# Optimization experiments

Hardware: AMD Instinct MI355X
Metric: run time of the kernel (lower is better)

The kernel has to match this reference:

```python
import jax, jax.numpy as jnp
import numpy as np

EMBED = 2048
HEADS = 32
HEAD_DIM = EMBED // HEADS
Q_BITS = 4
Q_MAX = 2 ** (Q_BITS - 1) - 1  # 7
DECOMP = 8
CHUNK = 256


def _sym_qdq(x, scale):
    # sym_quant followed by sym_dequant (float32 math, clamp to [-8, 7])
    s = jnp.clip(jnp.abs(scale), 1e-9, None)
    return jnp.clip(jnp.round(x / s), -(Q_MAX + 1), Q_MAX) * s


def _quant_weight(w):
    # per-output-channel symmetric int4 quant-dequant of weight [out, in]
    w = w.astype(jnp.float32)
    s = jnp.max(jnp.abs(w), axis=-1, keepdims=True) / Q_MAX
    return _sym_qdq(w, s)


def _chunk_decompose(x2d):
    """Tender chunked activation quantization.
    Splits rows into chunks of CHUNK, subtracts per-chunk channel bias,
    groups channels into DECOMP scale groups by their column max, and
    applies per-group int4 quant-dequant. Vectorized over the DECOMP groups
    (the masks partition channels, so a per-channel scale gather is exact).
    """
    T, H = x2d.shape
    chunks = (T + CHUNK - 1) // CHUNK
    pad = chunks * CHUNK - T
    xp = jnp.pad(x2d, ((0, pad), (0, 0))).reshape(chunks, CHUNK, H).astype(jnp.float32)
    ch_bias = (jnp.max(xp, axis=1, keepdims=True) + jnp.min(xp, axis=1, keepdims=True)) / 2
    xz = xp - ch_bias                                   # [chunks, CHUNK, H]
    tmax = jnp.max(jnp.abs(xz), axis=(1, 2))            # [chunks]
    cmax = jnp.max(jnp.abs(xz), axis=1)                 # [chunks, H]
    # thresholds t_i = tmax / 2^(DECOMP-1-i), ascending in i
    thr = tmax[:, None] / (2.0 ** jnp.arange(DECOMP - 1, -1, -1, dtype=jnp.float32))
    # group index: i=0 if cmax<=t0, else first i with t_{i-1} < cmax <= t_i
    idx = jnp.sum(cmax[:, :, None] > thr[:, None, : DECOMP - 1], axis=-1)  # [chunks, H]
    scale = tmax[:, None] / (2.0 ** (DECOMP - 1 - idx).astype(jnp.float32)) / Q_MAX
    result = _sym_qdq(xz, scale[:, None, :])            # [chunks, CHUNK, H]
    return result, ch_bias, T


def reference(hidden_states, q_weight, k_weight, v_weight, o_weight,
              q_bias, k_bias, v_bias, o_bias):
    bsz, tgt, H = hidden_states.shape
    # int4 dequantized weights, transposed for right-multiply
    WQ = _quant_weight(q_weight).T
    WK = _quant_weight(k_weight).T
    WV = _quant_weight(v_weight).T
    WO = _quant_weight(o_weight).T

    result, ch_bias, n = _chunk_decompose(hidden_states.reshape(bsz * tgt, H))

    def proj(w_orig, w_dq_t, b):
        # bias-corrected dequant GEMM: per-chunk channel bias uses the
        # ORIGINAL (fp) weight, quantized residual uses the int4 weight
        y = result @ w_dq_t + ch_bias @ w_orig.astype(jnp.float32).T
        return y.reshape(-1, H)[:n] + b

    scaling = HEAD_DIM ** -0.5
    Q = (proj(q_weight, WQ, q_bias) * scaling).reshape(bsz, tgt, HEADS, HEAD_DIM)
    K = proj(k_weight, WK, k_bias).reshape(bsz, tgt, HEADS, HEAD_DIM)
    V = proj(v_weight, WV, v_bias).reshape(bsz, tgt, HEADS, HEAD_DIM)

    # quant_mha == False path: plain attention
    attn = jnp.einsum('bqhd,bkhd->bhqk', Q, K)
    probs = jax.nn.softmax(attn, axis=-1)
    ctx = jnp.einsum('bhqk,bkhd->bqhd', probs, V).reshape(bsz * tgt, H)

    # output projection through the same chunked quant pipeline
    r2, cb2, n2 = _chunk_decompose(ctx)
    out = (r2 @ WO + cb2 @ o_weight.astype(jnp.float32).T).reshape(-1, H)[:n2] + o_bias
    return out.reshape(bsz, tgt, H)


def setup_inputs() -> dict:
    key = jax.random.key(0)
    ks = jax.random.split(key, 10)
    B, T = 2, 1024
    inp = {
        'hidden_states': jax.random.normal(ks[0], (B, T, EMBED), dtype=jnp.float32),
        'q_weight': jax.random.normal(ks[1], (EMBED, EMBED), dtype=jnp.float32) * 0.02,
        'k_weight': jax.random.normal(ks[2], (EMBED, EMBED), dtype=jnp.float32) * 0.02,
        'v_weight': jax.random.normal(ks[3], (EMBED, EMBED), dtype=jnp.float32) * 0.02,
        'o_weight': jax.random.normal(ks[4], (EMBED, EMBED), dtype=jnp.float32) * 0.02,
        'q_bias': jax.random.normal(ks[5], (EMBED,), dtype=jnp.float32) * 0.02,
        'k_bias': jax.random.normal(ks[6], (EMBED,), dtype=jnp.float32) * 0.02,
        'v_bias': jax.random.normal(ks[7], (EMBED,), dtype=jnp.float32) * 0.02,
        'o_bias': jax.random.normal(ks[8], (EMBED,), dtype=jnp.float32) * 0.02,
    }
    return inp
```

## Files before the change

kernel.cpp:

```cpp
#include <hip/hip_runtime.h>
#include <hip/hip_bf16.h>

typedef unsigned short u16;
typedef unsigned int u32;
typedef __attribute__((ext_vector_type(8))) short bs8;
typedef __attribute__((ext_vector_type(4))) float fx4;
typedef __attribute__((ext_vector_type(4))) float f4_t;
typedef __attribute__((ext_vector_type(4))) unsigned int u4_t;

#define HDIM 2048
#define NCH 8

__device__ inline u16 f2bf(float f) {
  __hip_bfloat16 h = __float2bfloat16(f);
  return __builtin_bit_cast(u16, h);
}
__device__ inline float bf2f(u16 u) {
  __hip_bfloat16 h = __builtin_bit_cast(__hip_bfloat16, u);
  return __bfloat162float(h);
}
__device__ inline float pow2i(int e) {
  return __builtin_bit_cast(float, (unsigned)((127 + e) << 23));
}
__device__ inline void gld_lds16(const void* g, void* l) {
  __builtin_amdgcn_global_load_lds((const __attribute__((address_space(1))) void*)g,
                                   (__attribute__((address_space(3))) void*)l, 16, 0, 0);
}

__global__ __launch_bounds__(256) void k_wquant_cbw(
    const float* __restrict__ w0, const float* __restrict__ w1,
    const float* __restrict__ w2, const float* __restrict__ bias,
    u16* __restrict__ wq, float* __restrict__ sw, float* __restrict__ cbw,
    int NC) {
  int o = blockIdx.x, t = threadIdx.x;
  const float* w = (o < 2048) ? w0 : ((o < 4096) ? w1 : w2);
  const float* wrow = w + (size_t)(o & 2047) * HDIM;
  const f4_t* row4 = (const f4_t*)wrow;
  f4_t x0 = row4[2 * t], x1 = row4[2 * t + 1];
  float am = 0.f;
#pragma unroll
  for (int j = 0; j < 4; j++) { am = fmaxf(am, fabsf(x0[j])); am = fmaxf(am, fabsf(x1[j])); }
#pragma unroll
  for (int m = 1; m < 64; m <<= 1) am = fmaxf(am, __shfl_xor(am, m));
  __shared__ float red[4];
  if ((t & 63) == 0) red[t >> 6] = am;
  __syncthreads();
  am = fmaxf(fmaxf(red[0], red[1]), fmaxf(red[2], red[3]));
  float s = fmaxf(am / 7.0f, 1e-9f);
  if (t == 0) sw[o] = s;
  bs8 ov;
#pragma unroll
  for (int j = 0; j < 4; j++) {
    float q0 = fminf(fmaxf(rintf(x0[j] / s), -8.f), 7.f);
    float q1 = fminf(fmaxf(rintf(x1[j] / s), -8.f), 7.f);
    ov[j]     = (short)f2bf(q0);
    ov[j + 4] = (short)f2bf(q1);
  }
  ((bs8*)(wq + (size_t)o * HDIM))[t] = ov;
  float acc[NCH];
#pragma unroll
  for (int c = 0; c < NCH; c++) {
    const f4_t* bc = (const f4_t*)(bias + (size_t)c * HDIM);
    f4_t b0 = bc[2 * t], b1 = bc[2 * t + 1];
    float a = 0.f;
#pragma unroll
    for (int j = 0; j < 4; j++) a += x0[j] * b0[j] + x1[j] * b1[j];
    acc[c] = a;
  }
  __shared__ float redc[NCH][4];
#pragma unroll
  for (int c = 0; c < NCH; c++) {
    float a = acc[c];
#pragma unroll
    for (int m = 1; m < 64; m <<= 1) a += __shfl_xor(a, m);
    if ((t & 63) == 0) redc[c][t >> 6] = a;
  }
  __syncthreads();
  if (t < NCH) cbw[t * NC + o] = redc[t][0] + redc[t][1] + redc[t][2] + redc[t][3];
}

__global__ __launch_bounds__(256) void k_stats(const float* __restrict__ x,
                                               float* __restrict__ biasO,
                                               float* __restrict__ cmaxO) {
  int ch = blockIdx.x >> 3;
  int c = ((blockIdx.x & 7) << 8) + threadIdx.x;
  const float* base = x + (size_t)ch * 256 * HDIM + c;
  float mx = -1e30f, mn = 1e30f;
  for (int r = 0; r < 256; r++) { float v = base[(size_t)r * HDIM]; mx = fmaxf(mx, v); mn = fminf(mn, v); }
  float bi = (mx + mn) * 0.5f;
  biasO[ch * HDIM + c] = bi;
  cmaxO[ch * HDIM + c] = fmaxf(mx - bi, bi - mn);
}

__global__ __launch_bounds__(256) void k_tscale(const float* __restrict__ cmax,
                                                float* __restrict__ scaleO,
                                                float* __restrict__ e2O,
                                                float* __restrict__ tcO) {
  int ch = blockIdx.x, t = threadIdx.x;
  const float* cr = cmax + ch * HDIM;
  float v[8];
  float mx = 0.f;
#pragma unroll
  for (int i = 0; i < 8; i++) { v[i] = cr[i * 256 + t]; mx = fmaxf(mx, v[i]); }
#pragma unroll
  for (int m = 1; m < 64; m <<= 1) mx = fmaxf(mx, __shfl_xor(mx, m));
  __shared__ float red[4];
  __shared__ float tms;
  if ((t & 63) == 0) red[t >> 6] = mx;
  __syncthreads();
  if (t == 0) tms = fmaxf(fmaxf(red[0], red[1]), fmaxf(red[2], red[3]));
  __syncthreads();
  float tmax = tms;
  if (t == 0) tcO[ch] = (tmax / 7.0f) * pow2i(-7);
#pragma unroll
  for (int i = 0; i < 8; i++) {
    int idx = 0;
#pragma unroll
    for (int k = 0; k < 7; k++) idx += (v[i] > tmax * pow2i(k - 7)) ? 1 : 0;
    float s = (tmax * pow2i(idx - 7)) / 7.0f;
    scaleO[ch * HDIM + i * 256 + t] = fmaxf(s, 1e-9f);
    e2O[ch * HDIM + i * 256 + t] = pow2i(idx);
  }
}

__global__ __launch_bounds__(256) void k_qdq(const float* __restrict__ x,
                                             const float* __restrict__ bias,
                                             const float* __restrict__ scale,
                                             const float* __restrict__ e2,
                                             u16* __restrict__ out) {
  int row = blockIdx.x, t = threadIdx.x;
  int ch = row >> 8;
  const f4_t* xr = (const f4_t*)(x + (size_t)row * HDIM);
  const f4_t* br = (const f4_t*)(bias + (size_t)ch * HDIM);
  const f4_t* sr = (const f4_t*)(scale + (size_t)ch * HDIM);
  const f4_t* er = (const f4_t*)(e2 + (size_t)ch * HDIM);
  f4_t x0 = xr[2 * t], x1 = xr[2 * t + 1];
  f4_t b0 = br[2 * t], b1 = br[2 * t + 1];
  f4_t s0 = sr[2 * t], s1 = sr[2 * t + 1];
  f4_t e0 = er[2 * t], e1 = er[2 * t + 1];
  bs8 ov;
#pragma unroll
  for (int j = 0; j < 4; j++) {
    float q0 = fminf(fmaxf(rintf((x0[j] - b0[j]) / s0[j]), -8.f), 7.f);
    ov[j] = (short)f2bf(q0 * e0[j]);
    float q1 = fminf(fmaxf(rintf((x1[j] - b1[j]) / s1[j]), -8.f), 7.f);
    ov[j + 4] = (short)f2bf(q1 * e1[j]);
  }
  ((bs8*)(out + (size_t)row * HDIM))[t] = ov;
}

__global__ __launch_bounds__(256) void k_gemm(
    const u16* __restrict__ A, const u16* __restrict__ B,
    float* __restrict__ o0, float* __restrict__ o1, float* __restrict__ o2,
    const float* __restrict__ cbw, int NC,
    const float* __restrict__ bb0, const float* __restrict__ bb1,
    const float* __restrict__ bb2,
    const float* __restrict__ tc, const float* __restrict__ sw,
    float scl0, float scl1, float scl2) {
  __shared__ u16 smA[128 * 32];
  __shared__ u16 smB[128 * 32];
  int tid = threadIdx.x;
  int wave = tid >> 6, lane = tid & 63;
  int wr = wave >> 1, wc = wave & 1;
  int row0 = blockIdx.y * 128, col0 = blockIdx.x * 128;
  int mat = col0 >> 11;
  float* out = (mat == 0) ? o0 : ((mat == 1) ? o1 : o2);
  const float* bias = (mat == 0) ? bb0 : ((mat == 1) ? bb1 : bb2);
  float scl = (mat == 0) ? scl0 : ((mat == 1) ? scl1 : scl2);
  int chunk = row0 >> 8;
  fx4 zz = {0.f, 0.f, 0.f, 0.f};
  fx4 acc[4][4];
#pragma unroll
  for (int m = 0; m < 4; m++)
#pragma unroll
    for (int n = 0; n < 4; n++) acc[m][n] = zz;

  int offB = wave * 1024 + lane * 16;
  int sr0 = offB >> 6;
  int sr1 = sr0 + 64;
  int sk = (lane & 3) << 3;
  char* ldsA0 = (char*)smA + wave * 1024;
  char* ldsA1 = (char*)smA + 4096 + wave * 1024;
  char* ldsB0 = (char*)smB + wave * 1024;
  char* ldsB1 = (char*)smB + 4096 + wave * 1024;
  const u16* Ab = A + (size_t)row0 * HDIM;
  const u16* Bb = B + (size_t)col0 * HDIM;

  int arow = wr * 64 + (lane & 15);
  int brow = wc * 64 + (lane & 15);
  int kByte = (lane >> 4) << 4;

  for (int kt = 0; kt < HDIM / 32; kt++) {
    int kb = kt * 32 + sk;
    gld_lds16(Ab + (size_t)sr0 * HDIM + kb, ldsA0);
    gld_lds16(Ab + (size_t)sr1 * HDIM + kb, ldsA1);
    gld_lds16(Bb + (size_t)sr0 * HDIM + kb, ldsB0);
    gld_lds16(Bb + (size_t)sr1 * HDIM + kb, ldsB1);
    __syncthreads();
    bs8 af[4], bfr[4];
#pragma unroll
    for (int m = 0; m < 4; m++)
      af[m] = *(const bs8*)((const char*)smA + (size_t)((arow + m * 16) * 64 + kByte));
#pragma unroll
    for (int n = 0; n < 4; n++)
      bfr[n] = *(const bs8*)((const char*)smB + (size_t)((brow + n * 16) * 64 + kByte));
#pragma unroll
    for (int m = 0; m < 4; m++)
#pragma unroll
      for (int n = 0; n < 4; n++)
        acc[m][n] = __builtin_amdgcn_mfma_f32_16x16x32_bf16(af[m], bfr[n], acc[m][n], 0, 0, 0);
    __syncthreads();
  }
  float tcv = tc[chunk];
  int colb = col0 + wc * 64 + (lane & 15);
  int rowb = row0 + wr * 64 + ((lane >> 4) << 2);
#pragma unroll
  for (int m = 0; m < 4; m++) {
#pragma unroll
    for (int n = 0; n < 4; n++) {
      int colg = colb + n * 16;
      int colL = colg - (mat << 11);
      float sc = tcv * sw[colg];
      float cb = cbw[chunk * NC + colg] + bias[colL];
#pragma unroll
      for (int j = 0; j < 4; j++) {
        int row = rowb + m * 16 + j;
        out[(size_t)row * HDIM + colL] = (acc[m][n][j] * sc + cb) * scl;
      }
    }
  }
}

__global__ __launch_bounds__(256) void k_gemm_sk(const u16* __restrict__ A,
                                                 const u16* __restrict__ B,
                                                 float* __restrict__ pbuf) {
  __shared__ u16 smA[128 * 32];
  __shared__ u16 smB[128 * 32];
  int tid = threadIdx.x;
  int wave = tid >> 6, lane = tid & 63;
  int wr = wave >> 1, wc = wave & 1;
  int row0 = blockIdx.y * 128, col0 = blockIdx.x * 128;
  int z = blockIdx.z;
  float* out = pbuf + (size_t)z * HDIM * HDIM;
  fx4 zz = {0.f, 0.f, 0.f, 0.f};
  fx4 acc[4][4];
#pragma unroll
  for (int m = 0; m < 4; m++)
#pragma unroll
    for (int n = 0; n < 4; n++) acc[m][n] = zz;

  int offB = wave * 1024 + lane * 16;
  int sr0 = offB >> 6;
  int sr1 = sr0 + 64;
  int sk = (lane & 3) << 3;
  char* ldsA0 = (char*)smA + wave * 1024;
  char* ldsA1 = (char*)smA + 4096 + wave * 1024;
  char* ldsB0 = (char*)smB + wave * 1024;
  char* ldsB1 = (char*)smB + 4096 + wave * 1024;
  const u16* Ab = A + (size_t)row0 * HDIM;
  const u16* Bb = B + (size_t)col0 * HDIM;

  int arow = wr * 64 + (lane & 15);
  int brow = wc * 64 + (lane & 15);
  int kByte = (lane >> 4) << 4;

  for (int kt = z * 32; kt < z * 32 + 32; kt++) {
    int kb = kt * 32 + sk;
    gld_lds16(Ab + (size_t)sr0 * HDIM + kb, ldsA0);
    gld_lds16(Ab + (size_t)sr1 * HDIM + kb, ldsA1);
    gld_lds16(Bb + (size_t)sr0 * HDIM + kb, ldsB0);
    gld_lds16(Bb + (size_t)sr1 * HDIM + kb, ldsB1);
    __syncthreads();
    bs8 af[4], bfr[4];
#pragma unroll
    for (int m = 0; m < 4; m++)
      af[m] = *(const bs8*)((const char*)smA + (size_t)((arow + m * 16) * 64 + kByte));
#pragma unroll
    for (int n = 0; n < 4; n++)
      bfr[n] = *(const bs8*)((const char*)smB + (size_t)((brow + n * 16) * 64 + kByte));
#pragma unroll
    for (int m = 0; m < 4; m++)
#pragma unroll
      for (int n = 0; n < 4; n++)
        acc[m][n] = __builtin_amdgcn_mfma_f32_16x16x32_bf16(af[m], bfr[n], acc[m][n], 0, 0, 0);
    __syncthreads();
  }
  int colb = col0 + wc * 64 + (lane & 15);
  int rowb = row0 + wr * 64 + ((lane >> 4) << 2);
#pragma unroll
  for (int m = 0; m < 4; m++)
#pragma unroll
    for (int n = 0; n < 4; n++)
#pragma unroll
      for (int j = 0; j < 4; j++)
        out[(size_t)(rowb + m * 16 + j) * HDIM + colb + n * 16] = acc[m][n][j];
}

__global__ __launch_bounds__(256) void k_fin(const float* __restrict__ p0,
                                             const float* __restrict__ p1,
                                             const float* __restrict__ cbw,
                                             const float* __restrict__ bias,
                                             const float* __restrict__ tc,
                                             const float* __restrict__ sw,
                                             float* __restrict__ out) {
  int row = blockIdx.x, t = threadIdx.x;
  int chunk = row >> 8;
  float tcv = tc[chunk];
  const f4_t* a = (const f4_t*)(p0 + (size_t)row * HDIM);
  const f4_t* b = (const f4_t*)(p1 + (size_t)row * HDIM);
  f4_t* o = (f4_t*)(out + (size_t)row * HDIM);
#pragma unroll
  for (int u = 0; u < 2; u++) {
    f4_t x = a[2 * t + u], y = b[2 * t + u];
    f4_t r;
#pragma unroll
    for (int j = 0; j < 4; j++) {
      int c = (2 * t + u) * 4 + j;
      float sc = tcv * sw[c];
      float cb = cbw[chunk * HDIM + c] + bias[c];
      r[j] = ((x[j] + y[j]) * sc + cb) * 1.0f;
    }
    o[2 * t + u] = r;
  }
}

__global__ __launch_bounds__(256) void k_split(const float* __restrict__ Kf,
                                               const float* __restrict__ Vf,
                                               u16* __restrict__ Khg,
                                               u16* __restrict__ Klg,
                                               u16* __restrict__ Vhg,
                                               u16* __restrict__ Vlg) {
  __shared__ u16 Th[4096], Tl[4096];
  int t = threadIdx.x;
  int ti = blockIdx.x & 15, h = (blockIdx.x >> 4) & 31, b = blockIdx.x >> 9;
  size_t rowStart = (size_t)b * 1024 + ti * 64;
  int colh = h * 64;
  size_t tbase = ((size_t)((b * 32 + h) * 16 + ti)) * 4096;
  int kr = t >> 2, d0 = (t & 3) << 4;
  int xk = (kr & 7) << 3;
  const float* kp = Kf + (rowStart + kr) * HDIM + colh + d0;
  const float* vp = Vf + (rowStart + kr) * HDIM + colh + d0;
  f4_t kv[4], vv[4];
#pragma unroll
  for (int qd = 0; qd < 4; qd++) { kv[qd] = *(const f4_t*)(kp + 4 * qd); vv[qd] = *(const f4_t*)(vp + 4 * qd); }
  bs8 h0, l0, h1, l1;
#pragma unroll
  for (int j = 0; j < 4; j++) {
    float x = kv[0][j]; u16 hh = f2bf(x); h0[j] = (short)hh; l0[j] = (short)f2bf(x - bf2f(hh));
    x = kv[1][j]; hh = f2bf(x); h0[j + 4] = (short)hh; l0[j + 4] = (short)f2bf(x - bf2f(hh));
    x = kv[2][j]; hh = f2bf(x); h1[j] = (short)hh; l1[j] = (short)f2bf(x - bf2f(hh));
    x = kv[3][j]; hh = f2bf(x); h1[j + 4] = (short)hh; l1[j + 4] = (short)f2bf(x - bf2f(hh));
  }
  *(bs8*)(Khg + tbase + kr * 64 + (d0 ^ xk)) = h0;
  *(bs8*)(Klg + tbase + kr * 64 + (d0 ^ xk)) = l0;
  *(bs8*)(Khg + tbase + kr * 64 + ((d0 + 8) ^ xk)) = h1;
  *(bs8*)(Klg + tbase + kr * 64 + ((d0 + 8) ^ xk)) = l1;
#pragma unroll
  for (int qd = 0; qd < 4; qd++)
#pragma unroll
    for (int j = 0; j < 4; j++) {
      int d = d0 + 4 * qd + j;
      float x = vv[qd][j]; u16 hh = f2bf(x);
      int vi = d * 64 + (kr ^ ((d & 7) << 3));
      Th[vi] = hh; Tl[vi] = f2bf(x - bf2f(hh));
    }
  __syncthreads();
  *(bs8*)(Vhg + tbase + t * 16) = *(const bs8*)&Th[t * 16];
  *(bs8*)(Vhg + tbase + t * 16 + 8) = *(const bs8*)&Th[t * 16 + 8];
  *(bs8*)(Vlg + tbase + t * 16) = *(const bs8*)&Tl[t * 16];
  *(bs8*)(Vlg + tbase + t * 16 + 8) = *(const bs8*)&Tl[t * 16 + 8];
}

__global__ __launch_bounds__(256) void k_attn(const float* __restrict__ Q,
                                              const u16* __restrict__ Khg,
                                              const u16* __restrict__ Klg,
                                              const u16* __restrict__ Vhg,
                                              const u16* __restrict__ Vlg,
                                              float* __restrict__ O) {
  __shared__ u16 Kh[64 * 64], Kl[64 * 64];
  __shared__ u16 Vh[64 * 64], Vl[64 * 64];
  int tid = threadIdx.x, wave = tid >> 6, lane = tid & 63;
  int l15 = lane & 15, l4 = lane >> 4;
  int lid = blockIdx.x;
  int xcd = lid & 7, jj = lid >> 3;
  int pair = xcd * 8 + (jj >> 4);
  int qt = jj & 15;
  int h = pair & 31, b = pair >> 5;
  size_t rowStart = (size_t)b * 1024;
  int colh = h * 64;
  int qbase = qt * 64 + wave * 16;
  size_t hbase = (size_t)pair * 16 * 4096;

  bs8 qh[2], ql[2];
#pragma unroll
  for (int kk = 0; kk < 2; kk++) {
    const float* qp = Q + (rowStart + qbase + l15) * HDIM + colh + kk * 32 + (l4 << 3);
    f4_t a0 = *(const f4_t*)qp;
    f4_t a1 = *(const f4_t*)(qp + 4);
#pragma unroll
    for (int j = 0; j < 4; j++) {
      float x = a0[j]; u16 hh = f2bf(x);
      qh[kk][j] = (short)hh; ql[kk][j] = (short)f2bf(x - bf2f(hh));
      x = a1[j]; hh = f2bf(x);
      qh[kk][j + 4] = (short)hh; ql[kk][j + 4] = (short)f2bf(x - bf2f(hh));
    }
  }

  fx4 zz = {0.f, 0.f, 0.f, 0.f};
  fx4 oacc[4];
  float mrun = -1e30f, lrun = 0.f;
#pragma unroll
  for (int n = 0; n < 4; n++) oacc[n] = zz;

  const u16* garr = (wave == 0) ? Khg : (wave == 1) ? Klg : (wave == 2) ? Vhg : Vlg;
  u16* larr = (wave == 0) ? Kh : (wave == 1) ? Kl : (wave == 2) ? Vh : Vl;

  int srcA = l15 + ((lane & 16) << 1);
  int srcB = srcA + 16;
  int hiSel = l4 >> 1;

  for (int ti = 0; ti < 16; ti++) {
    const u16* gsrc = garr + hbase + (size_t)ti * 4096 + lane * 8;
#pragma unroll
    for (int seg = 0; seg < 8; seg++)
      gld_lds16(gsrc + seg * 512, larr + seg * 512);
    __syncthreads();

    fx4 sf[4];
#pragma unroll
    for (int n = 0; n < 4; n++) sf[n] = zz;
    __builtin_amdgcn_s_setprio(1);
#pragma unroll
    for (int kk = 0; kk < 2; kk++) {
      int colr = kk * 32 + (l4 << 3);
#pragma unroll
      for (int n = 0; n < 4; n++) {
        int row = n * 16 + l15;
        int ko = row * 64 + (colr ^ ((row & 7) << 3));
        bs8 bh = *(const bs8*)&Kh[ko];
        bs8 bl = *(const bs8*)&Kl[ko];
        sf[n] = __builtin_amdgcn_mfma_f32_16x16x32_bf16(bl, ql[kk], sf[n], 0, 0, 0);
        sf[n] = __builtin_amdgcn_mfma_f32_16x16x32_bf16(bh, ql[kk], sf[n], 0, 0, 0);
        sf[n] = __builtin_amdgcn_mfma_f32_16x16x32_bf16(bl, qh[kk], sf[n], 0, 0, 0);
        sf[n] = __builtin_amdgcn_mfma_f32_16x16x32_bf16(bh, qh[kk], sf[n], 0, 0, 0);
      }
    }
    __builtin_amdgcn_s_setprio(0);
    float tm = sf[0][0];
#pragma unroll
    for (int n = 0; n < 4; n++)
#pragma unroll
      for (int j = 0; j < 4; j++) tm = fmaxf(tm, sf[n][j]);
    tm = fmaxf(tm, __shfl_xor(tm, 16));
    tm = fmaxf(tm, __shfl_xor(tm, 32));
    float mn = fmaxf(mrun, tm);
    float corr = __expf(mrun - mn);
    mrun = mn;
    float rs = 0.f;
#pragma unroll
    for (int n = 0; n < 4; n++)
#pragma unroll
      for (int j = 0; j < 4; j++) { float p = __expf(sf[n][j] - mn); sf[n][j] = p; rs += p; }
    rs += __shfl_xor(rs, 16);
    rs += __shfl_xor(rs, 32);
    lrun = lrun * corr + rs;
#pragma unroll
    for (int n = 0; n < 4; n++)
#pragma unroll
      for (int j = 0; j < 4; j++) oacc[n][j] *= corr;

    u32 hiw[4][2], low[4][2];
#pragma unroll
    for (int n = 0; n < 4; n++) {
      u16 hh0 = f2bf(sf[n][0]), hh1 = f2bf(sf[n][1]);
      u16 hh2 = f2bf(sf[n][2]), hh3 = f2bf(sf[n][3]);
      u16 ll0 = f2bf(sf[n][0] - bf2f(hh0)), ll1 = f2bf(sf[n][1] - bf2f(hh1));
      u16 ll2 = f2bf(sf[n][2] - bf2f(hh2)), ll3 = f2bf(sf[n][3] - bf2f(hh3));
      hiw[n][0] = (u32)hh0 | ((u32)hh1 << 16);
      hiw[n][1] = (u32)hh2 | ((u32)hh3 << 16);
      low[n][0] = (u32)ll0 | ((u32)ll1 << 16);
      low[n][1] = (u32)ll2 | ((u32)ll3 << 16);
    }
    bs8 ph[2], pl[2];
#pragma unroll
    for (int kkv = 0; kkv < 2; kkv++) {
      u4_t wh, wl;
#pragma unroll
      for (int half = 0; half < 2; half++) {
        int src = half ? srcB : srcA;
#pragma unroll
        for (int pr = 0; pr < 2; pr++) {
          int a0 = __shfl((int)hiw[2 * kkv][pr], src);
          int a1 = __shfl((int)hiw[2 * kkv + 1][pr], src);
          wh[half * 2 + pr] = (u32)(hiSel ? a1 : a0);
          int b0 = __shfl((int)low[2 * kkv][pr], src);
          int b1 = __shfl((int)low[2 * kkv + 1][pr], src);
          wl[half * 2 + pr] = (u32)(hiSel ? b1 : b0);
        }
      }
      ph[kkv] = __builtin_bit_cast(bs8, wh);
      pl[kkv] = __builtin_bit_cast(bs8, wl);
    }

    __builtin_amdgcn_s_setprio(1);
#pragma unroll
    for (int kkv = 0; kkv < 2; kkv++) {
      int colr = kkv * 32 + (l4 << 3);
#pragma unroll
      for (int n = 0; n < 4; n++) {
        int vrow = n * 16 + l15;
        int vo = vrow * 64 + (colr ^ ((vrow & 7) << 3));
        bs8 vh = *(const bs8*)&Vh[vo];
        bs8 vl = *(const bs8*)&Vl[vo];
        oacc[n] = __builtin_amdgcn_mfma_f32_16x16x32_bf16(vl, pl[kkv], oacc[n], 0, 0, 0);
        oacc[n] = __builtin_amdgcn_mfma_f32_16x16x32_bf16(vh, pl[kkv], oacc[n], 0, 0, 0);
        oacc[n] = __builtin_amdgcn_mfma_f32_16x16x32_bf16(vl, ph[kkv], oacc[n], 0, 0, 0);
        oacc[n] = __builtin_amdgcn_mfma_f32_16x16x32_bf16(vh, ph[kkv], oacc[n], 0, 0, 0);
      }
    }
    __builtin_amdgcn_s_setprio(0);
    __syncthreads();
  }
  size_t token = rowStart + qbase + l15;
#pragma unroll
  for (int n = 0; n < 4; n++) {
    f4_t r;
#pragma unroll
    for (int j = 0; j < 4; j++) r[j] = oacc[n][j] / lrun;
    *(f4_t*)(O + token * HDIM + colh + n * 16 + (l4 << 2)) = r;
  }
}

extern "C" void kernel_launch(void* const* d_in, const int* in_sizes, int n_in,
                              void* d_out, int out_size, void* d_ws, size_t ws_size,
                              hipStream_t stream) {
  const float* hs = (const float*)d_in[0];
  const float* qw = (const float*)d_in[1];
  const float* kw = (const float*)d_in[2];
  const float* vw = (const float*)d_in[3];
  const float* ow = (const float*)d_in[4];
  const float* qb = (const float*)d_in[5];
  const float* kb = (const float*)d_in[6];
  const float* vb = (const float*)d_in[7];
  const float* ob = (const float*)d_in[8];

  char* ws = (char*)d_ws;
  const size_t MB = 1u << 20;
  u16* wqQKV = (u16*)(ws + 0 * MB);
  u16* actA  = (u16*)(ws + 24 * MB);
  u16* Khg   = (u16*)(ws + 0 * MB);
  u16* Klg   = (u16*)(ws + 8 * MB);
  u16* Vhg   = (u16*)(ws + 16 * MB);
  u16* Vlg   = (u16*)(ws + 24 * MB);
  float* p01 = (float*)(ws + 0 * MB);
  float* Qf  = (float*)(ws + 32 * MB);
  float* Kf  = (float*)(ws + 48 * MB);
  float* Vf  = (float*)(ws + 64 * MB);
  u16* actA2 = (u16*)(ws + 48 * MB);
  u16* wqO   = (u16*)(ws + 64 * MB);
  float* sm  = (float*)(ws + 80 * MB);
  float* bias1  = sm;
  float* cmax1  = bias1 + NCH * HDIM;
  float* scale1 = cmax1 + NCH * HDIM;
  float* e2_1   = scale1 + NCH * HDIM;
  float* bias2  = e2_1 + NCH * HDIM;
  float* cmax2  = bias2 + NCH * HDIM;
  float* scale2 = cmax2 + NCH * HDIM;
  float* e2_2   = scale2 + NCH * HDIM;
  float* cbwQKV = e2_2 + NCH * HDIM;
  float* swQKV  = cbwQKV + NCH * 3 * HDIM;
  float* cbwO   = swQKV + 3 * HDIM;
  float* swO    = cbwO + NCH * HDIM;
  float* tc1    = swO + HDIM;
  float* tc2    = tc1 + NCH;
  float* ctx = (float*)d_out;

  k_stats<<<64, 256, 0, stream>>>(hs, bias1, cmax1);
  k_tscale<<<8, 256, 0, stream>>>(cmax1, scale1, e2_1, tc1);
  k_qdq<<<2048, 256, 0, stream>>>(hs, bias1, scale1, e2_1, actA);
  k_wquant_cbw<<<6144, 256, 0, stream>>>(qw, kw, vw, bias1, wqQKV, swQKV, cbwQKV, 3 * HDIM);
  k_gemm<<<dim3(48, 16), 256, 0, stream>>>(actA, wqQKV, Qf, Kf, Vf,
                                           cbwQKV, 3 * HDIM, qb, kb, vb,
                                           tc1, swQKV, 0.125f, 1.0f, 1.0f);
  k_split<<<1024, 256, 0, stream>>>(Kf, Vf, Khg, Klg, Vhg, Vlg);
  k_attn<<<1024, 256, 0, stream>>>(Qf, Khg, Klg, Vhg, Vlg, ctx);
  k_stats<<<64, 256, 0, stream>>>(ctx, bias2, cmax2);
  k_tscale<<<8, 256, 0, stream>>>(cmax2, scale2, e2_2, tc2);
  k_qdq<<<2048, 256, 0, stream>>>(ctx, bias2, scale2, e2_2, actA2);
  k_wquant_cbw<<<2048, 256, 0, stream>>>(ow, ow, ow, bias2, wqO, swO, cbwO, HDIM);
  k_gemm_sk<<<dim3(16, 16, 2), 256, 0, stream>>>(actA2, wqO, p01);
  k_fin<<<2048, 256, 0, stream>>>(p01, p01 + (size_t)HDIM * HDIM,
                                  cbwO, ob, tc2, swO, (float*)d_out);
}
```

Baseline: 294.7 us.

## Process two query tiles per attention block to reuse staged K/V tiles

```diff
diff --git a/kernel.cpp b/kernel.cpp
--- a/kernel.cpp
+++ b/kernel.cpp
@@ -383,34 +383,38 @@
   int l15 = lane & 15, l4 = lane >> 4;
   int lid = blockIdx.x;
   int xcd = lid & 7, jj = lid >> 3;
-  int pair = xcd * 8 + (jj >> 4);
-  int qt = jj & 15;
+  int pair = xcd * 8 + (jj >> 3);
+  int qt = jj & 7;
   int h = pair & 31, b = pair >> 5;
   size_t rowStart = (size_t)b * 1024;
   int colh = h * 64;
-  int qbase = qt * 64 + wave * 16;
   size_t hbase = (size_t)pair * 16 * 4096;
 
-  bs8 qh[2], ql[2];
-#pragma unroll
-  for (int kk = 0; kk < 2; kk++) {
-    const float* qp = Q + (rowStart + qbase + l15) * HDIM + colh + kk * 32 + (l4 << 3);
-    f4_t a0 = *(const f4_t*)qp;
-    f4_t a1 = *(const f4_t*)(qp + 4);
-#pragma unroll
-    for (int j = 0; j < 4; j++) {
-      float x = a0[j]; u16 hh = f2bf(x);
-      qh[kk][j] = (short)hh; ql[kk][j] = (short)f2bf(x - bf2f(hh));
-      x = a1[j]; hh = f2bf(x);
-      qh[kk][j + 4] = (short)hh; ql[kk][j + 4] = (short)f2bf(x - bf2f(hh));
-    }
-  }
+  bs8 qh[2][2], ql[2][2];
+#pragma unroll
+  for (int m = 0; m < 2; m++)
+#pragma unroll
+    for (int kk = 0; kk < 2; kk++) {
+      const float* qp = Q + (rowStart + qt * 128 + m * 64 + wave * 16 + l15) * HDIM +
+                        colh + kk * 32 + (l4 << 3);
+      f4_t a0 = *(const f4_t*)qp;
+      f4_t a1 = *(const f4_t*)(qp + 4);
+#pragma unroll
+      for (int j = 0; j < 4; j++) {
+        float x = a0[j]; u16 hh = f2bf(x);
+        qh[m][kk][j] = (short)hh; ql[m][kk][j] = (short)f2bf(x - bf2f(hh));
+        x = a1[j]; hh = f2bf(x);
+        qh[m][kk][j + 4] = (short)hh; ql[m][kk][j + 4] = (short)f2bf(x - bf2f(hh));
+      }
+    }
 
   fx4 zz = {0.f, 0.f, 0.f, 0.f};
-  fx4 oacc[4];
-  float mrun = -1e30f, lrun = 0.f;
-#pragma unroll
-  for (int n = 0; n < 4; n++) oacc[n] = zz;
+  fx4 oacc[2][4];
+  float mrun[2] = {-1e30f, -1e30f}, lrun[2] = {0.f, 0.f};
+#pragma unroll
+  for (int m = 0; m < 2; m++)
+#pragma unroll
+    for (int n = 0; n < 4; n++) oacc[m][n] = zz;
 
   const u16* garr = (wave == 0) ? Khg : (wave == 1) ? Klg : (wave == 2) ? Vhg : Vlg;
   u16* larr = (wave == 0) ? Kh : (wave == 1) ? Kl : (wave == 2) ? Vh : Vl;
@@ -426,9 +430,11 @@
       gld_lds16(gsrc + seg * 512, larr + seg * 512);
     __syncthreads();
 
-    fx4 sf[4];
-#pragma unroll
-    for (int n = 0; n < 4; n++) sf[n] = zz;
+    fx4 sf[2][4];
+#pragma unroll
+    for (int m = 0; m < 2; m++)
+#pragma unroll
+      for (int n = 0; n < 4; n++) sf[m][n] = zz;
     __builtin_amdgcn_s_setprio(1);
 #pragma unroll
     for (int kk = 0; kk < 2; kk++) {
@@ -439,67 +445,73 @@
         int ko = row * 64 + (colr ^ ((row & 7) << 3));
         bs8 bh = *(const bs8*)&Kh[ko];
         bs8 bl = *(const bs8*)&Kl[ko];
-        sf[n] = __builtin_amdgcn_mfma_f32_16x16x32_bf16(bl, ql[kk], sf[n], 0, 0, 0);
-        sf[n] = __builtin_amdgcn_mfma_f32_16x16x32_bf16(bh, ql[kk], sf[n], 0, 0, 0);
-        sf[n] = __builtin_amdgcn_mfma_f32_16x16x32_bf16(bl, qh[kk], sf[n], 0, 0, 0);
-        sf[n] = __builtin_amdgcn_mfma_f32_16x16x32_bf16(bh, qh[kk], sf[n], 0, 0, 0);
-      }
-    }
-    __builtin_amdgcn_s_setprio(0);
-    float tm = sf[0][0];
-#pragma unroll
-    for (int n = 0; n < 4; n++)
-#pragma unroll
-      for (int j = 0; j < 4; j++) tm = fmaxf(tm, sf[n][j]);
-    tm = fmaxf(tm, __shfl_xor(tm, 16));
-    tm = fmaxf(tm, __shfl_xor(tm, 32));
-    float mn = fmaxf(mrun, tm);
-    float corr = __expf(mrun - mn);
-    mrun = mn;
-    float rs = 0.f;
-#pragma unroll
-    for (int n = 0; n < 4; n++)
-#pragma unroll
-      for (int j = 0; j < 4; j++) { float p = __expf(sf[n][j] - mn); sf[n][j] = p; rs += p; }
-    rs += __shfl_xor(rs, 16);
-    rs += __shfl_xor(rs, 32);
-    lrun = lrun * corr + rs;
-#pragma unroll
-    for (int n = 0; n < 4; n++)
-#pragma unroll
-      for (int j = 0; j < 4; j++) oacc[n][j] *= corr;
-
-    u32 hiw[4][2], low[4][2];
-#pragma unroll
-    for (int n = 0; n < 4; n++) {
-      u16 hh0 = f2bf(sf[n][0]), hh1 = f2bf(sf[n][1]);
-      u16 hh2 = f2bf(sf[n][2]), hh3 = f2bf(sf[n][3]);
-      u16 ll0 = f2bf(sf[n][0] - bf2f(hh0)), ll1 = f2bf(sf[n][1] - bf2f(hh1));
-      u16 ll2 = f2bf(sf[n][2] - bf2f(hh2)), ll3 = f2bf(sf[n][3] - bf2f(hh3));
-      hiw[n][0] = (u32)hh0 | ((u32)hh1 << 16);
-      hiw[n][1] = (u32)hh2 | ((u32)hh3 << 16);
-      low[n][0] = (u32)ll0 | ((u32)ll1 << 16);
-      low[n][1] = (u32)ll2 | ((u32)ll3 << 16);
-    }
-    bs8 ph[2], pl[2];
-#pragma unroll
-    for (int kkv = 0; kkv < 2; kkv++) {
-      u4_t wh, wl;
-#pragma unroll
-      for (int half = 0; half < 2; half++) {
-        int src = half ? srcB : srcA;
-#pragma unroll
-        for (int pr = 0; pr < 2; pr++) {
-          int a0 = __shfl((int)hiw[2 * kkv][pr], src);
-          int a1 = __shfl((int)hiw[2 * kkv + 1][pr], src);
-          wh[half * 2 + pr] = (u32)(hiSel ? a1 : a0);
-          int b0 = __shfl((int)low[2 * kkv][pr], src);
-          int b1 = __shfl((int)low[2 * kkv + 1][pr], src);
-          wl[half * 2 + pr] = (u32)(hiSel ? b1 : b0);
+#pragma unroll
+        for (int m = 0; m < 2; m++) {
+          sf[m][n] = __builtin_amdgcn_mfma_f32_16x16x32_bf16(bl, ql[m][kk], sf[m][n], 0, 0, 0);
+          sf[m][n] = __builtin_amdgcn_mfma_f32_16x16x32_bf16(bh, ql[m][kk], sf[m][n], 0, 0, 0);
+          sf[m][n] = __builtin_amdgcn_mfma_f32_16x16x32_bf16(bl, qh[m][kk], sf[m][n], 0, 0, 0);
+          sf[m][n] = __builtin_amdgcn_mfma_f32_16x16x32_bf16(bh, qh[m][kk], sf[m][n], 0, 0, 0);
         }
       }
-      ph[kkv] = __builtin_bit_cast(bs8, wh);
-      pl[kkv] = __builtin_bit_cast(bs8, wl);
+    }
+    __builtin_amdgcn_s_setprio(0);
+    bs8 ph[2][2], pl[2][2];
+#pragma unroll
+    for (int m = 0; m < 2; m++) {
+      float tm = sf[m][0][0];
+#pragma unroll
+      for (int n = 0; n < 4; n++)
+#pragma unroll
+        for (int j = 0; j < 4; j++) tm = fmaxf(tm, sf[m][n][j]);
+      tm = fmaxf(tm, __shfl_xor(tm, 16));
+      tm = fmaxf(tm, __shfl_xor(tm, 32));
+      float mn = fmaxf(mrun[m], tm);
+      float corr = __expf(mrun[m] - mn);
+      mrun[m] = mn;
+      float rs = 0.f;
+#pragma unroll
+      for (int n = 0; n < 4; n++)
+#pragma unroll
+        for (int j = 0; j < 4; j++) { float p = __expf(sf[m][n][j] - mn); sf[m][n][j] = p; rs += p; }
+      rs += __shfl_xor(rs, 16);
+      rs += __shfl_xor(rs, 32);
+      lrun[m] = lrun[m] * corr + rs;
+#pragma unroll
+      for (int n = 0; n < 4; n++)
+#pragma unroll
+        for (int j = 0; j < 4; j++) oacc[m][n][j] *= corr;
+
+      u32 hiw[4][2], low[4][2];
+#pragma unroll
+      for (int n = 0; n < 4; n++) {
+        u16 hh0 = f2bf(sf[m][n][0]), hh1 = f2bf(sf[m][n][1]);
+        u16 hh2 = f2bf(sf[m][n][2]), hh3 = f2bf(sf[m][n][3]);
+        u16 ll0 = f2bf(sf[m][n][0] - bf2f(hh0)), ll1 = f2bf(sf[m][n][1] - bf2f(hh1));
+        u16 ll2 = f2bf(sf[m][n][2] - bf2f(hh2)), ll3 = f2bf(sf[m][n][3] - bf2f(hh3));
+        hiw[n][0] = (u32)hh0 | ((u32)hh1 << 16);
+        hiw[n][1] = (u32)hh2 | ((u32)hh3 << 16);
+        low[n][0] = (u32)ll0 | ((u32)ll1 << 16);
+        low[n][1] = (u32)ll2 | ((u32)ll3 << 16);
+      }
+#pragma unroll
+      for (int kkv = 0; kkv < 2; kkv++) {
+        u4_t wh, wl;
+#pragma unroll
+        for (int half = 0; half < 2; half++) {
+          int src = half ? srcB : srcA;
+#pragma unroll
+          for (int pr = 0; pr < 2; pr++) {
+            int a0 = __shfl((int)hiw[2 * kkv][pr], src);
+            int a1 = __shfl((int)hiw[2 * kkv + 1][pr], src);
+            wh[half * 2 + pr] = (u32)(hiSel ? a1 : a0);
+            int b0 = __shfl((int)low[2 * kkv][pr], src);
+            int b1 = __shfl((int)low[2 * kkv + 1][pr], src);
+            wl[half * 2 + pr] = (u32)(hiSel ? b1 : b0);
+          }
+        }
+        ph[m][kkv] = __builtin_bit_cast(bs8, wh);
+        pl[m][kkv] = __builtin_bit_cast(bs8, wl);
+      }
     }
 
     __builtin_amdgcn_s_setprio(1);
@@ -512,22 +524,28 @@
         int vo = vrow * 64 + (colr ^ ((vrow & 7) << 3));
         bs8 vh = *(const bs8*)&Vh[vo];
         bs8 vl = *(const bs8*)&Vl[vo];
-        oacc[n] = __builtin_amdgcn_mfma_f32_16x16x32_bf16(vl, pl[kkv], oacc[n], 0, 0, 0);
-        oacc[n] = __builtin_amdgcn_mfma_f32_16x16x32_bf16(vh, pl[kkv], oacc[n], 0, 0, 0);
-        oacc[n] = __builtin_amdgcn_mfma_f32_16x16x32_bf16(vl, ph[kkv], oacc[n], 0, 0, 0);
-        oacc[n] = __builtin_amdgcn_mfma_f32_16x16x32_bf16(vh, ph[kkv], oacc[n], 0, 0, 0);
+#pragma unroll
+        for (int m = 0; m < 2; m++) {
+          oacc[m][n] = __builtin_amdgcn_mfma_f32_16x16x32_bf16(vl, pl[m][kkv], oacc[m][n], 0, 0, 0);
+          oacc[m][n] = __builtin_amdgcn_mfma_f32_16x16x32_bf16(vh, pl[m][kkv], oacc[m][n], 0, 0, 0);
+          oacc[m][n] = __builtin_amdgcn_mfma_f32_16x16x32_bf16(vl, ph[m][kkv], oacc[m][n], 0, 0, 0);
+          oacc[m][n] = __builtin_amdgcn_mfma_f32_16x16x32_bf16(vh, ph[m][kkv], oacc[m][n], 0, 0, 0);
+        }
       }
     }
     __builtin_amdgcn_s_setprio(0);
     __syncthreads();
   }
-  size_t token = rowStart + qbase + l15;
-#pragma unroll
-  for (int n = 0; n < 4; n++) {
-    f4_t r;
-#pragma unroll
-    for (int j = 0; j < 4; j++) r[j] = oacc[n][j] / lrun;
-    *(f4_t*)(O + token * HDIM + colh + n * 16 + (l4 << 2)) = r;
+#pragma unroll
+  for (int m = 0; m < 2; m++) {
+    size_t token = rowStart + qt * 128 + m * 64 + wave * 16 + l15;
+#pragma unroll
+    for (int n = 0; n < 4; n++) {
+      f4_t r;
+#pragma unroll
+      for (int j = 0; j < 4; j++) r[j] = oacc[m][n][j] / lrun[m];
+      *(f4_t*)(O + token * HDIM + colh + n * 16 + (l4 << 2)) = r;
+    }
   }
 }
 
@@ -583,7 +601,7 @@
                                            cbwQKV, 3 * HDIM, qb, kb, vb,
                                            tc1, swQKV, 0.125f, 1.0f, 1.0f);
   k_split<<<1024, 256, 0, stream>>>(Kf, Vf, Khg, Klg, Vhg, Vlg);
-  k_attn<<<1024, 256, 0, stream>>>(Qf, Khg, Klg, Vhg, Vlg, ctx);
+  k_attn<<<512, 256, 0, stream>>>(Qf, Khg, Klg, Vhg, Vlg, ctx);
   k_stats<<<64, 256, 0, stream>>>(ctx, bias2, cmax2);
   k_tscale<<<8, 256, 0, stream>>>(cmax2, scale2, e2_2, tc2);
   k_qdq<<<2048, 256, 0, stream>>>(ctx, bias2, scale2, e2_2, actA2);
```

After: 297.9 us. Within noise of the previous version (+1.1%).

## Read attention K/V tiles directly from global memory and use three-way split-K

Applied to the files above, without the earlier changes.

```diff
diff --git a/kernel.cpp b/kernel.cpp
--- a/kernel.cpp
+++ b/kernel.cpp
@@ -233,7 +233,9 @@
 
 __global__ __launch_bounds__(256) void k_gemm_sk(const u16* __restrict__ A,
                                                  const u16* __restrict__ B,
-                                                 float* __restrict__ pbuf) {
+                                                 float* __restrict__ p0,
+                                                 float* __restrict__ p1,
+                                                 float* __restrict__ p2) {
   __shared__ u16 smA[128 * 32];
   __shared__ u16 smB[128 * 32];
   int tid = threadIdx.x;
@@ -241,7 +243,9 @@
   int wr = wave >> 1, wc = wave & 1;
   int row0 = blockIdx.y * 128, col0 = blockIdx.x * 128;
   int z = blockIdx.z;
-  float* out = pbuf + (size_t)z * HDIM * HDIM;
+  float* out = (z == 0) ? p0 : ((z == 1) ? p1 : p2);
+  int kt0 = 21 * z;
+  int kt1 = (z == 2) ? 64 : (21 * z + 21);
   fx4 zz = {0.f, 0.f, 0.f, 0.f};
   fx4 acc[4][4];
 #pragma unroll
@@ -264,7 +268,7 @@
   int brow = wc * 64 + (lane & 15);
   int kByte = (lane >> 4) << 4;
 
-  for (int kt = z * 32; kt < z * 32 + 32; kt++) {
+  for (int kt = kt0; kt < kt1; kt++) {
     int kb = kt * 32 + sk;
     gld_lds16(Ab + (size_t)sr0 * HDIM + kb, ldsA0);
     gld_lds16(Ab + (size_t)sr1 * HDIM + kb, ldsA1);
@@ -298,6 +302,7 @@
 
 __global__ __launch_bounds__(256) void k_fin(const float* __restrict__ p0,
                                              const float* __restrict__ p1,
+                                             const float* __restrict__ p2,
                                              const float* __restrict__ cbw,
                                              const float* __restrict__ bias,
                                              const float* __restrict__ tc,
@@ -308,17 +313,18 @@
   float tcv = tc[chunk];
   const f4_t* a = (const f4_t*)(p0 + (size_t)row * HDIM);
   const f4_t* b = (const f4_t*)(p1 + (size_t)row * HDIM);
+  const f4_t* c_ = (const f4_t*)(p2 + (size_t)row * HDIM);
   f4_t* o = (f4_t*)(out + (size_t)row * HDIM);
 #pragma unroll
   for (int u = 0; u < 2; u++) {
-    f4_t x = a[2 * t + u], y = b[2 * t + u];
+    f4_t x = a[2 * t + u], y = b[2 * t + u], w = c_[2 * t + u];
     f4_t r;
 #pragma unroll
     for (int j = 0; j < 4; j++) {
       int c = (2 * t + u) * 4 + j;
       float sc = tcv * sw[c];
       float cb = cbw[chunk * HDIM + c] + bias[c];
-      r[j] = ((x[j] + y[j]) * sc + cb) * 1.0f;
+      r[j] = ((x[j] + y[j] + w[j]) * sc + cb) * 1.0f;
     }
     o[2 * t + u] = r;
   }
@@ -377,8 +383,6 @@
                                               const u16* __restrict__ Vhg,
                                               const u16* __restrict__ Vlg,
                                               float* __restrict__ O) {
-  __shared__ u16 Kh[64 * 64], Kl[64 * 64];
-  __shared__ u16 Vh[64 * 64], Vl[64 * 64];
   int tid = threadIdx.x, wave = tid >> 6, lane = tid & 63;
   int l15 = lane & 15, l4 = lane >> 4;
   int lid = blockIdx.x;
@@ -412,19 +416,15 @@
 #pragma unroll
   for (int n = 0; n < 4; n++) oacc[n] = zz;
 
-  const u16* garr = (wave == 0) ? Khg : (wave == 1) ? Klg : (wave == 2) ? Vhg : Vlg;
-  u16* larr = (wave == 0) ? Kh : (wave == 1) ? Kl : (wave == 2) ? Vh : Vl;
-
   int srcA = l15 + ((lane & 16) << 1);
   int srcB = srcA + 16;
   int hiSel = l4 >> 1;
 
   for (int ti = 0; ti < 16; ti++) {
-    const u16* gsrc = garr + hbase + (size_t)ti * 4096 + lane * 8;
-#pragma unroll
-    for (int seg = 0; seg < 8; seg++)
-      gld_lds16(gsrc + seg * 512, larr + seg * 512);
-    __syncthreads();
+    const u16* KhT = Khg + hbase + (size_t)ti * 4096;
+    const u16* KlT = Klg + hbase + (size_t)ti * 4096;
+    const u16* VhT = Vhg + hbase + (size_t)ti * 4096;
+    const u16* VlT = Vlg + hbase + (size_t)ti * 4096;
 
     fx4 sf[4];
 #pragma unroll
@@ -437,8 +437,8 @@
       for (int n = 0; n < 4; n++) {
         int row = n * 16 + l15;
         int ko = row * 64 + (colr ^ ((row & 7) << 3));
-        bs8 bh = *(const bs8*)&Kh[ko];
-        bs8 bl = *(const bs8*)&Kl[ko];
+        bs8 bh = *(const bs8*)(KhT + ko);
+        bs8 bl = *(const bs8*)(KlT + ko);
         sf[n] = __builtin_amdgcn_mfma_f32_16x16x32_bf16(bl, ql[kk], sf[n], 0, 0, 0);
         sf[n] = __builtin_amdgcn_mfma_f32_16x16x32_bf16(bh, ql[kk], sf[n], 0, 0, 0);
         sf[n] = __builtin_amdgcn_mfma_f32_16x16x32_bf16(bl, qh[kk], sf[n], 0, 0, 0);
@@ -510,8 +510,8 @@
       for (int n = 0; n < 4; n++) {
         int vrow = n * 16 + l15;
         int vo = vrow * 64 + (colr ^ ((vrow & 7) << 3));
-        bs8 vh = *(const bs8*)&Vh[vo];
-        bs8 vl = *(const bs8*)&Vl[vo];
+        bs8 vh = *(const bs8*)(VhT + vo);
+        bs8 vl = *(const bs8*)(VlT + vo);
         oacc[n] = __builtin_amdgcn_mfma_f32_16x16x32_bf16(vl, pl[kkv], oacc[n], 0, 0, 0);
         oacc[n] = __builtin_amdgcn_mfma_f32_16x16x32_bf16(vh, pl[kkv], oacc[n], 0, 0, 0);
         oacc[n] = __builtin_amdgcn_mfma_f32_16x16x32_bf16(vl, ph[kkv], oacc[n], 0, 0, 0);
@@ -519,7 +519,6 @@
       }
     }
     __builtin_amdgcn_s_setprio(0);
-    __syncthreads();
   }
   size_t token = rowStart + qbase + l15;
 #pragma unroll
@@ -552,7 +551,8 @@
   u16* Klg   = (u16*)(ws + 8 * MB);
   u16* Vhg   = (u16*)(ws + 16 * MB);
   u16* Vlg   = (u16*)(ws + 24 * MB);
-  float* p01 = (float*)(ws + 0 * MB);
+  float* p0  = (float*)(ws + 0 * MB);
+  float* p1  = (float*)(ws + 16 * MB);
   float* Qf  = (float*)(ws + 32 * MB);
   float* Kf  = (float*)(ws + 48 * MB);
   float* Vf  = (float*)(ws + 64 * MB);
@@ -574,6 +574,7 @@
   float* tc1    = swO + HDIM;
   float* tc2    = tc1 + NCH;
   float* ctx = (float*)d_out;
+  float* p2  = (float*)d_out;
 
   k_stats<<<64, 256, 0, stream>>>(hs, bias1, cmax1);
   k_tscale<<<8, 256, 0, stream>>>(cmax1, scale1, e2_1, tc1);
@@ -588,7 +589,6 @@
   k_tscale<<<8, 256, 0, stream>>>(cmax2, scale2, e2_2, tc2);
   k_qdq<<<2048, 256, 0, stream>>>(ctx, bias2, scale2, e2_2, actA2);
   k_wquant_cbw<<<2048, 256, 0, stream>>>(ow, ow, ow, bias2, wqO, swO, cbwO, HDIM);
-  k_gemm_sk<<<dim3(16, 16, 2), 256, 0, stream>>>(actA2, wqO, p01);
-  k_fin<<<2048, 256, 0, stream>>>(p01, p01 + (size_t)HDIM * HDIM,
-                                  cbwO, ob, tc2, swO, (float*)d_out);
-}
+  k_gemm_sk<<<dim3(16, 16, 3), 256, 0, stream>>>(actA2, wqO, p0, p1, p2);
+  k_fin<<<2048, 256, 0, stream>>>(p0, p1, p2, cbwO, ob, tc2, swO, (float*)d_out);
+}
```

Result: slower. 330.8 us (+12.3%).

## Double GEMM K-tile to 64 with XOR-swizzled LDS layout

Applied to the files above, without the earlier changes.

```diff
diff --git a/kernel.cpp b/kernel.cpp
--- a/kernel.cpp
+++ b/kernel.cpp
@@ -156,9 +156,9 @@
     const float* __restrict__ bb0, const float* __restrict__ bb1,
     const float* __restrict__ bb2,
     const float* __restrict__ tc, const float* __restrict__ sw,
-    float scl0, float scl1, float scl2) {
-  __shared__ u16 smA[128 * 32];
-  __shared__ u16 smB[128 * 32];
+    float scl0, float scl1, float scl2, int kt0, int kt1) {
+  __shared__ u16 smA[128 * 64];
+  __shared__ u16 smB[128 * 64];
   int tid = threadIdx.x;
   int wave = tid >> 6, lane = tid & 63;
   int wr = wave >> 1, wc = wave & 1;
@@ -175,41 +175,47 @@
 #pragma unroll
     for (int n = 0; n < 4; n++) acc[m][n] = zz;
 
-  int offB = wave * 1024 + lane * 16;
-  int sr0 = offB >> 6;
-  int sr1 = sr0 + 64;
-  int sk = (lane & 3) << 3;
-  char* ldsA0 = (char*)smA + wave * 1024;
-  char* ldsA1 = (char*)smA + 4096 + wave * 1024;
-  char* ldsB0 = (char*)smB + wave * 1024;
-  char* ldsB1 = (char*)smB + 4096 + wave * 1024;
+  int srow = wave * 8 + (lane >> 3);
+  int scol = (((lane & 7) ^ (lane >> 3)) << 3);
   const u16* Ab = A + (size_t)row0 * HDIM;
   const u16* Bb = B + (size_t)col0 * HDIM;
 
   int arow = wr * 64 + (lane & 15);
   int brow = wc * 64 + (lane & 15);
-  int kByte = (lane >> 4) << 4;
-
-  for (int kt = 0; kt < HDIM / 32; kt++) {
-    int kb = kt * 32 + sk;
-    gld_lds16(Ab + (size_t)sr0 * HDIM + kb, ldsA0);
-    gld_lds16(Ab + (size_t)sr1 * HDIM + kb, ldsA1);
-    gld_lds16(Bb + (size_t)sr0 * HDIM + kb, ldsB0);
-    gld_lds16(Bb + (size_t)sr1 * HDIM + kb, ldsB1);
+  int xA = (arow & 7) << 4;
+  int xB = (brow & 7) << 4;
+  int kB0 = (lane >> 4) << 4;
+
+  for (int kt = kt0; kt < kt1; kt++) {
+    int kb = kt * 64 + scol;
+#pragma unroll
+    for (int r = 0; r < 4; r++) {
+      gld_lds16(Ab + (size_t)(r * 32 + srow) * HDIM + kb,
+                (char*)smA + (r * 32 + wave * 8) * 128);
+      gld_lds16(Bb + (size_t)(r * 32 + srow) * HDIM + kb,
+                (char*)smB + (r * 32 + wave * 8) * 128);
+    }
     __syncthreads();
-    bs8 af[4], bfr[4];
-#pragma unroll
-    for (int m = 0; m < 4; m++)
-      af[m] = *(const bs8*)((const char*)smA + (size_t)((arow + m * 16) * 64 + kByte));
-#pragma unroll
-    for (int n = 0; n < 4; n++)
-      bfr[n] = *(const bs8*)((const char*)smB + (size_t)((brow + n * 16) * 64 + kByte));
-#pragma unroll
-    for (int m = 0; m < 4; m++)
+#pragma unroll
+    for (int kk = 0; kk < 2; kk++) {
+      bs8 af[4], bfr[4];
+#pragma unroll
+      for (int m = 0; m < 4; m++)
+        af[m] = *(const bs8*)((const char*)smA + (size_t)((arow + m * 16) * 128 +
+                                ((kk * 64 + kB0) ^ xA)));
 #pragma unroll
       for (int n = 0; n < 4; n++)
-        acc[m][n] = __builtin_amdgcn_mfma_f32_16x16x32_bf16(af[m], bfr[n], acc[m][n], 0, 0, 0);
+        bfr[n] = *(const bs8*)((const char*)smB + (size_t)((brow + n * 16) * 128 +
+                                ((kk * 64 + kB0) ^ xB)));
+#pragma unroll
+      for (int m = 0; m < 4; m++)
+#pragma unroll
+        for (int n = 0; n < 4; n++)
+          acc[m][n] = __builtin_amdgcn_mfma_f32_16x16x32_bf16(af[m], bfr[n], acc[m][n], 0, 0, 0);
+    }
     __syncthreads();
+  }
+  if (o0 == nullptr) {
   }
   float tcv = tc[chunk];
   int colb = col0 + wc * 64 + (lane & 15);
@@ -234,8 +240,8 @@
 __global__ __launch_bounds__(256) void k_gemm_sk(const u16* __restrict__ A,
                                                  const u16* __restrict__ B,
                                                  float* __restrict__ pbuf) {
-  __shared__ u16 smA[128 * 32];
-  __shared__ u16 smB[128 * 32];
+  __shared__ u16 smA[128 * 64];
+  __shared__ u16 smB[128 * 64];
   int tid = threadIdx.x;
   int wave = tid >> 6, lane = tid & 63;
   int wr = wave >> 1, wc = wave & 1;
@@ -249,40 +255,44 @@
 #pragma unroll
     for (int n = 0; n < 4; n++) acc[m][n] = zz;
 
-  int offB = wave * 1024 + lane * 16;
-  int sr0 = offB >> 6;
-  int sr1 = sr0 + 64;
-  int sk = (lane & 3) << 3;
-  char* ldsA0 = (char*)smA + wave * 1024;
-  char* ldsA1 = (char*)smA + 4096 + wave * 1024;
-  char* ldsB0 = (char*)smB + wave * 1024;
-  char* ldsB1 = (char*)smB + 4096 + wave * 1024;
+  int srow = wave * 8 + (lane >> 3);
+  int scol = (((lane & 7) ^ (lane >> 3)) << 3);
   const u16* Ab = A + (size_t)row0 * HDIM;
   const u16* Bb = B + (size_t)col0 * HDIM;
 
   int arow = wr * 64 + (lane & 15);
   int brow = wc * 64 + (lane & 15);
-  int kByte = (lane >> 4) << 4;
-
-  for (int kt = z * 32; kt < z * 32 + 32; kt++) {
-    int kb = kt * 32 + sk;
-    gld_lds16(Ab + (size_t)sr0 * HDIM + kb, ldsA0);
-    gld_lds16(Ab + (size_t)sr1 * HDIM + kb, ldsA1);
-    gld_lds16(Bb + (size_t)sr0 * HDIM + kb, ldsB0);
-    gld_lds16(Bb + (size_t)sr1 * HDIM + kb, ldsB1);
+  int xA = (arow & 7) << 4;
+  int xB = (brow & 7) << 4;
+  int kB0 = (lane >> 4) << 4;
+
+  for (int kt = z * 16; kt < z * 16 + 16; kt++) {
+    int kb = kt * 64 + scol;
+#pragma unroll
+    for (int r = 0; r < 4; r++) {
+      gld_lds16(Ab + (size_t)(r * 32 + srow) * HDIM + kb,
+                (char*)smA + (r * 32 + wave * 8) * 128);
+      gld_lds16(Bb + (size_t)(r * 32 + srow) * HDIM + kb,
+                (char*)smB + (r * 32 + wave * 8) * 128);
+    }
     __syncthreads();
-    bs8 af[4], bfr[4];
-#pragma unroll
-    for (int m = 0; m < 4; m++)
-      af[m] = *(const bs8*)((const char*)smA + (size_t)((arow + m * 16) * 64 + kByte));
-#pragma unroll
-    for (int n = 0; n < 4; n++)
-      bfr[n] = *(const bs8*)((const char*)smB + (size_t)((brow + n * 16) * 64 + kByte));
-#pragma unroll
-    for (int m = 0; m < 4; m++)
+#pragma unroll
+    for (int kk = 0; kk < 2; kk++) {
+      bs8 af[4], bfr[4];
+#pragma unroll
+      for (int m = 0; m < 4; m++)
+        af[m] = *(const bs8*)((const char*)smA + (size_t)((arow + m * 16) * 128 +
+                                ((kk * 64 + kB0) ^ xA)));
 #pragma unroll
       for (int n = 0; n < 4; n++)
-        acc[m][n] = __builtin_amdgcn_mfma_f32_16x16x32_bf16(af[m], bfr[n], acc[m][n], 0, 0, 0);
+        bfr[n] = *(const bs8*)((const char*)smB + (size_t)((brow + n * 16) * 128 +
+                                ((kk * 64 + kB0) ^ xB)));
+#pragma unroll
+      for (int m = 0; m < 4; m++)
+#pragma unroll
+        for (int n = 0; n < 4; n++)
+          acc[m][n] = __builtin_amdgcn_mfma_f32_16x16x32_bf16(af[m], bfr[n], acc[m][n], 0, 0, 0);
+    }
     __syncthreads();
   }
   int colb = col0 + wc * 64 + (lane & 15);
@@ -581,7 +591,7 @@
   k_wquant_cbw<<<6144, 256, 0, stream>>>(qw, kw, vw, bias1, wqQKV, swQKV, cbwQKV, 3 * HDIM);
   k_gemm<<<dim3(48, 16), 256, 0, stream>>>(actA, wqQKV, Qf, Kf, Vf,
                                            cbwQKV, 3 * HDIM, qb, kb, vb,
-                                           tc1, swQKV, 0.125f, 1.0f, 1.0f);
+                                           tc1, swQKV, 0.125f, 1.0f, 1.0f, 0, 32);
   k_split<<<1024, 256, 0, stream>>>(Kf, Vf, Khg, Klg, Vhg, Vlg);
   k_attn<<<1024, 256, 0, stream>>>(Qf, Khg, Klg, Vhg, Vlg, ctx);
   k_stats<<<64, 256, 0, stream>>>(ctx, bias2, cmax2);
```

Result: faster. 281.2 us (-4.6%).
